# Kernel optimization log

Measured on AMD Instinct MI355X. Metric: run time of the kernel, lower is better.

## Reference

```python
import jax, jax.numpy as jnp
import numpy as np

EPS = 1e-6
R = 8


def _gram_schmidt(U, eps=EPS):
    # Modified Gram-Schmidt over the r columns of U (dim, r), matching the
    # sequential projection loop in HouseholderReflection.get_orthogonal_matrix.
    cols = []
    u0 = U[:, 0]
    cols.append(u0 / (jnp.linalg.norm(u0) + eps))
    r = U.shape[1]
    for i in range(1, r):
        ui = U[:, i]
        for j in range(i):
            ui = ui - jnp.dot(cols[j], ui) * cols[j]
        cols.append(ui / (jnp.linalg.norm(ui) + eps))
    return cols  # list of r unit vectors (dim,)


def _orthogonal_matrix(hra_u, eps=EPS):
    # Q = prod_i (I - 2 u_i u_i^T), applied as rank-1 updates: Q <- Q - 2 (Q u) u^T
    dim = hra_u.shape[0]
    cols = _gram_schmidt(hra_u, eps)
    Q = jnp.eye(dim, dtype=hra_u.dtype)
    for u in cols:
        Q = Q - 2.0 * jnp.outer(Q @ u, u)
    return Q  # (dim, dim)


def setup_inputs() -> dict:
    key = jax.random.key(0)
    k1, k2, k3, k4, k5 = jax.random.split(key, 5)
    N, D_IN, D_HID, D_OUT = 4096, 2048, 8192, 2048
    x = jax.random.normal(k1, (N, D_IN), dtype=jnp.float32)
    hra_u = jax.random.normal(k2, (D_IN, R), dtype=jnp.float32)
    W_random = jax.random.normal(k3, (D_IN, D_HID), dtype=jnp.float32) / np.sqrt(D_IN)
    W_out = jax.random.normal(k4, (D_HID, D_OUT), dtype=jnp.float32) / np.sqrt(D_HID)
    bias = jax.random.normal(k5, (D_OUT,), dtype=jnp.float32)
    return {"x": x, "hra_u": hra_u, "W_random": W_random, "W_out": W_out, "bias": bias}


def reference(x, hra_u, W_random, W_out, bias):
    # y = gelu(x @ (Q @ W_random)) @ W_out + bias  (torch nn.GELU = exact erf gelu)
    Q = _orthogonal_matrix(hra_u)
    W_t = Q @ W_random                      # (D_IN, D_HID)
    h = jax.nn.gelu(x @ W_t, approximate=False)  # (N, D_HID)
    return h @ W_out + bias                 # (N, D_OUT)
```

## Files before the change

kernel.cpp:

```cpp
#include <hip/hip_runtime.h>
#include <hip/hip_bf16.h>

typedef __bf16 bf16;
typedef __bf16 bf16x4 __attribute__((ext_vector_type(4)));
typedef __bf16 bf16x8 __attribute__((ext_vector_type(8)));
typedef float  f32x4  __attribute__((ext_vector_type(4)));

#define GAS __attribute__((address_space(1)))
#define LAS __attribute__((address_space(3)))

#define NROWS 4096
#define DIN   2048
#define DHID  8192
#define DOUT  2048

__device__ __forceinline__ void gload16(const void* g, void* l) {
    __builtin_amdgcn_global_load_lds((GAS void*)g, (LAS void*)l, 16, 0, 0);
}
template <int N> __device__ __forceinline__ void vmw() {
    asm volatile("s_waitcnt vmcnt(%0)" :: "n"(N) : "memory");
}
__device__ __forceinline__ void bsync() {
    asm volatile("" ::: "memory");
    __builtin_amdgcn_s_barrier();
    asm volatile("" ::: "memory");
}

__global__ __launch_bounds__(64) void gs_kernel(const float* __restrict__ U,
                                                float* __restrict__ Vt) {
    __shared__ float Vs[8][DIN];
    const int l = threadIdx.x;
    float u[32];
    for (int r = 0; r < 8; ++r) {
        #pragma unroll
        for (int s = 0; s < 32; ++s) u[s] = U[(size_t)(l * 32 + s) * 8 + r];
        for (int j = 0; j < r; ++j) {
            float d = 0.f;
            #pragma unroll
            for (int s = 0; s < 32; ++s) d += Vs[j][l * 32 + s] * u[s];
            #pragma unroll
            for (int o = 32; o >= 1; o >>= 1) d += __shfl_xor(d, o);
            #pragma unroll
            for (int s = 0; s < 32; ++s) u[s] -= d * Vs[j][l * 32 + s];
        }
        float nr = 0.f;
        #pragma unroll
        for (int s = 0; s < 32; ++s) nr += u[s] * u[s];
        #pragma unroll
        for (int o = 32; o >= 1; o >>= 1) nr += __shfl_xor(nr, o);
        const float inv = 1.f / (sqrtf(nr) + 1e-6f);
        #pragma unroll
        for (int s = 0; s < 32; ++s) {
            float v = u[s] * inv;
            Vs[r][l * 32 + s] = v;
            Vt[r * DIN + l * 32 + s] = v;
        }
        __syncthreads();
    }
}

__global__ __launch_bounds__(256) void p_kernel(const float* __restrict__ W,
                                                const float* __restrict__ Vt,
                                                float* __restrict__ P) {
    const int t = threadIdx.x;
    const int c = blockIdx.x * 64 + (t & 63);
    const int part = t >> 6;
    float acc[8] = {};
    const int i0 = part * 512;
    #pragma unroll 4
    for (int i = i0; i < i0 + 512; ++i) {
        float w = W[(size_t)i * DHID + c];
        #pragma unroll
        for (int r = 0; r < 8; ++r) acc[r] = fmaf(Vt[r * DIN + i], w, acc[r]);
    }
    __shared__ float red[4][8][64];
    #pragma unroll
    for (int r = 0; r < 8; ++r) red[part][r][t & 63] = acc[r];
    __syncthreads();
    for (int idx = t; idx < 512; idx += 256) {
        int r = idx >> 6, cc = idx & 63;
        P[(size_t)r * DHID + blockIdx.x * 64 + cc] =
            red[0][r][cc] + red[1][r][cc] + red[2][r][cc] + red[3][r][cc];
    }
}

__global__ __launch_bounds__(64) void xv_kernel(const float* __restrict__ x,
                                                const float* __restrict__ Vt,
                                                float* __restrict__ xV) {
    const int row = blockIdx.x, l = threadIdx.x;
    const float* xr = x + (size_t)row * DIN;
    float acc[8] = {};
    #pragma unroll 4
    for (int s = 0; s < 32; ++s) {
        int k = s * 64 + l;
        float xv = xr[k];
        #pragma unroll
        for (int r = 0; r < 8; ++r) acc[r] = fmaf(xv, Vt[r * DIN + k], acc[r]);
    }
    #pragma unroll
    for (int r = 0; r < 8; ++r) {
        float d = acc[r];
        #pragma unroll
        for (int o = 32; o >= 1; o >>= 1) d += __shfl_xor(d, o);
        if (l == 0) xV[(size_t)row * 8 + r] = d;
    }
}

__global__ __launch_bounds__(256) void conv_kernel(const float* __restrict__ in,
                                                   bf16* __restrict__ out, int n4) {
    int i = blockIdx.x * 256 + threadIdx.x;
    int stride = gridDim.x * 256;
    for (; i < n4; i += stride) {
        float4 v = ((const float4*)in)[i];
        bf16x4 o = { (bf16)v.x, (bf16)v.y, (bf16)v.z, (bf16)v.w };
        *(bf16x4*)&out[(size_t)i * 4] = o;
    }
}

__global__ __launch_bounds__(256) void tconv_kernel(const float* __restrict__ in,
                                                    bf16* __restrict__ out,
                                                    int R, int C) {
    __shared__ bf16 tile[64][66];
    const int t = threadIdx.x;
    const int n0 = blockIdx.x * 64, k0 = blockIdx.y * 64;
    const int rr = t >> 4, c4 = (t & 15) * 4;
    #pragma unroll
    for (int q = 0; q < 4; ++q) {
        int row = k0 + rr + q * 16;
        float4 v = *(const float4*)&in[(size_t)row * C + n0 + c4];
        tile[c4 + 0][rr + q * 16] = (bf16)v.x;
        tile[c4 + 1][rr + q * 16] = (bf16)v.y;
        tile[c4 + 2][rr + q * 16] = (bf16)v.z;
        tile[c4 + 3][rr + q * 16] = (bf16)v.w;
    }
    __syncthreads();
    const int n = t >> 2, kk = (t & 3) * 16;
    unsigned int w[8];
    #pragma unroll
    for (int i = 0; i < 8; ++i) w[i] = *(const unsigned int*)&tile[n][kk + i * 2];
    uint4 lo = { w[0], w[1], w[2], w[3] }, hi = { w[4], w[5], w[6], w[7] };
    uint4* dst = (uint4*)&out[(size_t)(n0 + n) * R + k0 + kk];
    dst[0] = lo;
    dst[1] = hi;
}

template <int BM, int BN, int WM, int WN, int CR, int CC, int EPI>
__global__ __launch_bounds__(512) void gemm256(const bf16* __restrict__ A,
                                               const bf16* __restrict__ Bt,
                                               const int N, const int K,
                                               const float* __restrict__ e0,
                                               const float* __restrict__ e1,
                                               void* __restrict__ Cout) {
    constexpr int MF = BM / (WM * 16);
    constexpr int NF = BN / (WN * 16);
    constexpr int ABYTES = BM * 64;
    constexpr int BUFB = (BM + BN) * 64;
    constexpr int LA = BM / 128, LB = BN / 128, LPT = LA + LB;
    __shared__ __align__(128) char lds[4 * BUFB];

    const int t = threadIdx.x;
    const int wid = t >> 6, lane = t & 63;
    const int wr = wid / WN, wc = wid % WN;
    const int lrow = lane & 15;
    const int lk2 = (lane >> 4) * 16;

    const int chunks_c = (N / BN) / CC;
    const int xc = blockIdx.x & 7;
    const int ii = blockIdx.x >> 3;
    const int bm = (xc / chunks_c) * CR + ii / CC;
    const int bn = (xc % chunks_c) * CC + ii % CC;

    const bf16* Abase = A + (size_t)bm * BM * K;
    const bf16* Bbase = Bt + (size_t)bn * BN * K;

    const int ar0 = wr * (MF * 16) + lrow;
    const unsigned aoff = (unsigned)(ar0 * 64 + lk2) ^ (unsigned)(((ar0 >> 1) & 3) << 4);
    const int br0 = wc * (NF * 16) + lrow;
    const unsigned boff = (unsigned)ABYTES +
        ((unsigned)(br0 * 64 + lk2) ^ (unsigned)(((br0 >> 1) & 3) << 4));

    f32x4 acc[MF][NF] = {};

    auto STAGE = [&](int kt, int b) {
        const size_t ko = (size_t)kt * 32;
        char* dstb = lds + b * BUFB;
        #pragma unroll
        for (int i2 = 0; i2 < LA; ++i2) {
            const int lin = i2 * 512 + t;
            const int row = lin >> 2;
            const int c16 = (lin & 3) ^ ((lin >> 3) & 3);
            gload16(Abase + (size_t)row * K + ko + c16 * 8,
                    dstb + (i2 * 512 + (t & 448)) * 16);
        }
        #pragma unroll
        for (int i2 = 0; i2 < LB; ++i2) {
            const int lin = i2 * 512 + t;
            const int row = lin >> 2;
            const int c16 = (lin & 3) ^ ((lin >> 3) & 3);
            gload16(Bbase + (size_t)row * K + ko + c16 * 8,
                    dstb + ABYTES + (i2 * 512 + (t & 448)) * 16);
        }
    };

    auto COMPUTE = [&](int b) {
        const char* bp = lds + b * BUFB;
        bf16x8 af[MF], bv[NF];
        #pragma unroll
        for (int m = 0; m < MF; ++m) af[m] = *(const bf16x8*)(bp + aoff + m * 1024);
        #pragma unroll
        for (int n = 0; n < NF; ++n) bv[n] = *(const bf16x8*)(bp + boff + n * 1024);
        __builtin_amdgcn_s_setprio(1);
        #pragma unroll
        for (int m = 0; m < MF; ++m)
            #pragma unroll
            for (int n = 0; n < NF; ++n)
                acc[m][n] = __builtin_amdgcn_mfma_f32_16x16x32_bf16(af[m], bv[n], acc[m][n], 0, 0, 0);
        __builtin_amdgcn_s_setprio(0);
    };

    const int nk = K >> 5;
    STAGE(0, 0); STAGE(1, 1); STAGE(2, 2);
    int kt = 0;
    for (; kt < nk - 3; ++kt) {
        STAGE(kt + 3, (kt + 3) & 3);
        vmw<3 * LPT>();
        bsync();
        COMPUTE(kt & 3);
        bsync();
    }
    vmw<2 * LPT>(); bsync(); COMPUTE(kt & 3); bsync(); ++kt;
    vmw<1 * LPT>(); bsync(); COMPUTE(kt & 3); bsync(); ++kt;
    vmw<0>();       bsync(); COMPUTE(kt & 3); bsync();

    const int jrow = (lane >> 4) << 2;
    if (EPI == 1) {
        float* xVl = (float*)lds;
        float* Pl  = (float*)(lds + BM * 32);
        for (int idx = t; idx < BM * 8; idx += 512)
            xVl[idx] = e0[((size_t)bm * BM + (idx >> 3)) * 8 + (idx & 7)];
        for (int idx = t; idx < BN * 8; idx += 512)
            Pl[idx] = e1[(size_t)(idx / BN) * N + (size_t)bn * BN + (idx % BN)];
        bsync();
        bf16* outp = (bf16*)Cout;
        #pragma unroll
        for (int m = 0; m < MF; ++m)
            #pragma unroll
            for (int n = 0; n < NF; ++n)
                #pragma unroll
                for (int j = 0; j < 4; ++j) {
                    const int rl = wr * (MF * 16) + m * 16 + jrow + j;
                    const int cl = wc * (NF * 16) + n * 16 + lrow;
                    float v = acc[m][n][j];
                    float corr = 0.f;
                    #pragma unroll
                    for (int r = 0; r < 8; ++r)
                        corr = fmaf(xVl[rl * 8 + r], Pl[r * BN + cl], corr);
                    v = fmaf(-2.f, corr, v);
                    v = 0.5f * v * (1.f + erff(v * 0.70710678118654752440f));
                    outp[((size_t)bm * BM + rl) * N + bn * BN + cl] = (bf16)v;
                }
    } else {
        float* outp = (float*)Cout;
        #pragma unroll
        for (int m = 0; m < MF; ++m)
            #pragma unroll
            for (int n = 0; n < NF; ++n)
                #pragma unroll
                for (int j = 0; j < 4; ++j) {
                    const int rl = wr * (MF * 16) + m * 16 + jrow + j;
                    const int cl = wc * (NF * 16) + n * 16 + lrow;
                    outp[((size_t)bm * BM + rl) * N + bn * BN + cl] =
                        acc[m][n][j] + e0[bn * BN + cl];
                }
    }
}

extern "C" void kernel_launch(void* const* d_in, const int* in_sizes, int n_in,
                              void* d_out, int out_size, void* d_ws, size_t ws_size,
                              hipStream_t stream) {
    const float* x     = (const float*)d_in[0];
    const float* hra_u = (const float*)d_in[1];
    const float* Wr    = (const float*)d_in[2];
    const float* Wo    = (const float*)d_in[3];
    const float* bias  = (const float*)d_in[4];
    float* out = (float*)d_out;
    char* ws = (char*)d_ws;

    float* Vt  = (float*)(ws + 0);
    float* P   = (float*)(ws + 65536);
    float* xV  = (float*)(ws + 327680);
    bf16*  xb  = (bf16*)(ws + 458752);
    bf16*  WrT = (bf16*)(ws + 17235968);
    bf16*  WoT = (bf16*)(ws + 50790400);
    bf16*  hb  = (bf16*)(ws + 84344832);

    gs_kernel<<<dim3(1), dim3(64), 0, stream>>>(hra_u, Vt);
    p_kernel<<<dim3(DHID / 64), dim3(256), 0, stream>>>(Wr, Vt, P);
    xv_kernel<<<dim3(NROWS), dim3(64), 0, stream>>>(x, Vt, xV);
    conv_kernel<<<dim3(2048), dim3(256), 0, stream>>>(x, xb, (NROWS * DIN) / 4);
    tconv_kernel<<<dim3(DHID / 64, DIN / 64), dim3(256), 0, stream>>>(Wr, WrT, DIN, DHID);
    tconv_kernel<<<dim3(DOUT / 64, DHID / 64), dim3(256), 0, stream>>>(Wo, WoT, DHID, DOUT);

    gemm256<256, 256, 2, 4, 8, 8, 1><<<dim3(512), dim3(512), 0, stream>>>(
        xb, WrT, DHID, DIN, xV, P, (void*)hb);
    gemm256<256, 128, 4, 2, 4, 8, 0><<<dim3(256), dim3(512), 0, stream>>>(
        hb, WoT, DOUT, DHID, bias, nullptr, (void*)out);
}
```

Baseline: 635.6 us.

## Split GEMM K-loop into half-tile stages, split-K the output GEMM, fuse bf16 conversion

The GEMM main loop now issues the next tile's global-to-LDS loads in two halves (A, then B), each interleaved with half of the MFMA work and separated by barriers. The goal is to overlap memory traffic with compute more finely and to remove the separate pre-compute wait and sync. The second GEMM switches to 256x256 tiles with a 2-way split-K: one half writes to the output, the other to a scratch buffer, and a new reduction kernel adds the two halves plus the bias. That costs an extra full-size fp32 read/write pass. Separately, the x-to-bf16 conversion is merged into the xV projection kernel, which now uses vectorised loads, so x is read once instead of twice.

```diff
diff --git a/kernel.cpp b/kernel.cpp
--- a/kernel.cpp
+++ b/kernel.cpp
@@ -84,18 +84,26 @@
     }
 }
 
-__global__ __launch_bounds__(64) void xv_kernel(const float* __restrict__ x,
-                                                const float* __restrict__ Vt,
-                                                float* __restrict__ xV) {
-    const int row = blockIdx.x, l = threadIdx.x;
+__global__ __launch_bounds__(256) void xv_kernel(const float* __restrict__ x,
+                                                 const float* __restrict__ Vt,
+                                                 float* __restrict__ xV,
+                                                 bf16* __restrict__ xb) {
+    const int row = blockIdx.x * 4 + (threadIdx.x >> 6);
+    const int l = threadIdx.x & 63;
     const float* xr = x + (size_t)row * DIN;
+    bf16* xbr = xb + (size_t)row * DIN;
     float acc[8] = {};
-    #pragma unroll 4
-    for (int s = 0; s < 32; ++s) {
-        int k = s * 64 + l;
-        float xv = xr[k];
-        #pragma unroll
-        for (int r = 0; r < 8; ++r) acc[r] = fmaf(xv, Vt[r * DIN + k], acc[r]);
+    #pragma unroll
+    for (int s = 0; s < 8; ++s) {
+        const int c0 = (s * 64 + l) * 4;
+        float4 v = *(const float4*)&xr[c0];
+        bf16x4 o = { (bf16)v.x, (bf16)v.y, (bf16)v.z, (bf16)v.w };
+        *(bf16x4*)&xbr[c0] = o;
+        #pragma unroll
+        for (int r = 0; r < 8; ++r) {
+            float4 vt = *(const float4*)&Vt[r * DIN + c0];
+            acc[r] = fmaf(v.x, vt.x, fmaf(v.y, vt.y, fmaf(v.z, vt.z, fmaf(v.w, vt.w, acc[r]))));
+        }
     }
     #pragma unroll
     for (int r = 0; r < 8; ++r) {
@@ -103,17 +111,6 @@
         #pragma unroll
         for (int o = 32; o >= 1; o >>= 1) d += __shfl_xor(d, o);
         if (l == 0) xV[(size_t)row * 8 + r] = d;
-    }
-}
-
-__global__ __launch_bounds__(256) void conv_kernel(const float* __restrict__ in,
-                                                   bf16* __restrict__ out, int n4) {
-    int i = blockIdx.x * 256 + threadIdx.x;
-    int stride = gridDim.x * 256;
-    for (; i < n4; i += stride) {
-        float4 v = ((const float4*)in)[i];
-        bf16x4 o = { (bf16)v.x, (bf16)v.y, (bf16)v.z, (bf16)v.w };
-        *(bf16x4*)&out[(size_t)i * 4] = o;
     }
 }
 
@@ -144,13 +141,26 @@
     dst[1] = hi;
 }
 
+__global__ __launch_bounds__(256) void redk(float* __restrict__ out,
+                                            const float* __restrict__ p1,
+                                            const float* __restrict__ bias) {
+    const size_t i = (size_t)blockIdx.x * 256 + threadIdx.x;
+    float4 a = ((const float4*)out)[i];
+    float4 b = ((const float4*)p1)[i];
+    const int c4 = (int)(i & (DOUT / 4 - 1)) * 4;
+    float4 bb = *(const float4*)&bias[c4];
+    float4 r = { a.x + b.x + bb.x, a.y + b.y + bb.y,
+                 a.z + b.z + bb.z, a.w + b.w + bb.w };
+    ((float4*)out)[i] = r;
+}
+
 template <int BM, int BN, int WM, int WN, int CR, int CC, int EPI>
-__global__ __launch_bounds__(512) void gemm256(const bf16* __restrict__ A,
-                                               const bf16* __restrict__ Bt,
-                                               const int N, const int K,
-                                               const float* __restrict__ e0,
-                                               const float* __restrict__ e1,
-                                               void* __restrict__ Cout) {
+__global__ __launch_bounds__(512) void gemm8p(const bf16* __restrict__ A,
+                                              const bf16* __restrict__ Bt,
+                                              const int N, const int nk, const int lda,
+                                              const float* __restrict__ e0,
+                                              const float* __restrict__ e1,
+                                              void* __restrict__ Cout) {
     constexpr int MF = BM / (WM * 16);
     constexpr int NF = BN / (WN * 16);
     constexpr int ABYTES = BM * 64;
@@ -164,14 +174,17 @@
     const int lrow = lane & 15;
     const int lk2 = (lane >> 4) * 16;
 
+    int bid = blockIdx.x, sk = 0;
+    if constexpr (EPI == 2) { sk = bid & 1; bid >>= 1; }
     const int chunks_c = (N / BN) / CC;
-    const int xc = blockIdx.x & 7;
-    const int ii = blockIdx.x >> 3;
+    const int xc = bid & 7;
+    const int ii = bid >> 3;
     const int bm = (xc / chunks_c) * CR + ii / CC;
     const int bn = (xc % chunks_c) * CC + ii % CC;
 
-    const bf16* Abase = A + (size_t)bm * BM * K;
-    const bf16* Bbase = Bt + (size_t)bn * BN * K;
+    const size_t koff = (size_t)sk * nk * 32;
+    const bf16* Abase = A + (size_t)bm * BM * lda + koff;
+    const bf16* Bbase = Bt + (size_t)bn * BN * lda + koff;
 
     const int ar0 = wr * (MF * 16) + lrow;
     const unsigned aoff = (unsigned)(ar0 * 64 + lk2) ^ (unsigned)(((ar0 >> 1) & 3) << 4);
@@ -181,59 +194,80 @@
 
     f32x4 acc[MF][NF] = {};
 
-    auto STAGE = [&](int kt, int b) {
+    auto STAGE = [&](int kt, int part) {
         const size_t ko = (size_t)kt * 32;
-        char* dstb = lds + b * BUFB;
-        #pragma unroll
-        for (int i2 = 0; i2 < LA; ++i2) {
-            const int lin = i2 * 512 + t;
-            const int row = lin >> 2;
-            const int c16 = (lin & 3) ^ ((lin >> 3) & 3);
-            gload16(Abase + (size_t)row * K + ko + c16 * 8,
-                    dstb + (i2 * 512 + (t & 448)) * 16);
-        }
-        #pragma unroll
-        for (int i2 = 0; i2 < LB; ++i2) {
-            const int lin = i2 * 512 + t;
-            const int row = lin >> 2;
-            const int c16 = (lin & 3) ^ ((lin >> 3) & 3);
-            gload16(Bbase + (size_t)row * K + ko + c16 * 8,
-                    dstb + ABYTES + (i2 * 512 + (t & 448)) * 16);
+        char* dstb = lds + (kt & 3) * BUFB;
+        if (part == 0) {
+            #pragma unroll
+            for (int i2 = 0; i2 < LA; ++i2) {
+                const int lin = i2 * 512 + t;
+                const int row = lin >> 2;
+                const int c16 = (lin & 3) ^ ((lin >> 3) & 3);
+                gload16(Abase + (size_t)row * lda + ko + c16 * 8,
+                        dstb + (i2 * 512 + (t & 448)) * 16);
+            }
+        } else {
+            #pragma unroll
+            for (int i2 = 0; i2 < LB; ++i2) {
+                const int lin = i2 * 512 + t;
+                const int row = lin >> 2;
+                const int c16 = (lin & 3) ^ ((lin >> 3) & 3);
+                gload16(Bbase + (size_t)row * lda + ko + c16 * 8,
+                        dstb + ABYTES + (i2 * 512 + (t & 448)) * 16);
+            }
         }
     };
 
-    auto COMPUTE = [&](int b) {
-        const char* bp = lds + b * BUFB;
-        bf16x8 af[MF], bv[NF];
-        #pragma unroll
-        for (int m = 0; m < MF; ++m) af[m] = *(const bf16x8*)(bp + aoff + m * 1024);
-        #pragma unroll
-        for (int n = 0; n < NF; ++n) bv[n] = *(const bf16x8*)(bp + boff + n * 1024);
+    auto TILE = [&](int kt, bool dostage) {
+        const char* bp = lds + (kt & 3) * BUFB;
+        bf16x8 av0[MF / 2], av1[MF / 2], bv[NF];
+        #pragma unroll
+        for (int m = 0; m < MF / 2; ++m)
+            av0[m] = *(const bf16x8*)(bp + aoff + m * 1024);
+        #pragma unroll
+        for (int n = 0; n < NF; ++n)
+            bv[n] = *(const bf16x8*)(bp + boff + n * 1024);
+        if (dostage) STAGE(kt + 3, 0);
+        __builtin_amdgcn_sched_barrier(0);
+        bsync();
         __builtin_amdgcn_s_setprio(1);
         #pragma unroll
-        for (int m = 0; m < MF; ++m)
+        for (int m = 0; m < MF / 2; ++m)
             #pragma unroll
             for (int n = 0; n < NF; ++n)
-                acc[m][n] = __builtin_amdgcn_mfma_f32_16x16x32_bf16(af[m], bv[n], acc[m][n], 0, 0, 0);
+                acc[m][n] = __builtin_amdgcn_mfma_f32_16x16x32_bf16(av0[m], bv[n], acc[m][n], 0, 0, 0);
+        __builtin_amdgcn_s_setprio(0);
+        bsync();
+        #pragma unroll
+        for (int m = 0; m < MF / 2; ++m)
+            av1[m] = *(const bf16x8*)(bp + aoff + (m + MF / 2) * 1024);
+        if (dostage) STAGE(kt + 3, 1);
+        __builtin_amdgcn_sched_barrier(0);
+        bsync();
+        __builtin_amdgcn_s_setprio(1);
+        #pragma unroll
+        for (int m = 0; m < MF / 2; ++m)
+            #pragma unroll
+            for (int n = 0; n < NF; ++n)
+                acc[m + MF / 2][n] = __builtin_amdgcn_mfma_f32_16x16x32_bf16(av1[m], bv[n], acc[m + MF / 2][n], 0, 0, 0);
         __builtin_amdgcn_s_setprio(0);
     };
 
-    const int nk = K >> 5;
-    STAGE(0, 0); STAGE(1, 1); STAGE(2, 2);
+    #pragma unroll
+    for (int p = 0; p < 3; ++p) { STAGE(p, 0); STAGE(p, 1); }
+    vmw<2 * LPT>(); bsync();
     int kt = 0;
     for (; kt < nk - 3; ++kt) {
-        STAGE(kt + 3, (kt + 3) & 3);
-        vmw<3 * LPT>();
-        bsync();
-        COMPUTE(kt & 3);
-        bsync();
-    }
-    vmw<2 * LPT>(); bsync(); COMPUTE(kt & 3); bsync(); ++kt;
-    vmw<1 * LPT>(); bsync(); COMPUTE(kt & 3); bsync(); ++kt;
-    vmw<0>();       bsync(); COMPUTE(kt & 3); bsync();
+        TILE(kt, true);
+        vmw<2 * LPT>();
+        bsync();
+    }
+    TILE(kt, false); vmw<LPT>(); bsync(); ++kt;
+    TILE(kt, false); vmw<0>();   bsync(); ++kt;
+    TILE(kt, false); bsync();
 
     const int jrow = (lane >> 4) << 2;
-    if (EPI == 1) {
+    if constexpr (EPI == 1) {
         float* xVl = (float*)lds;
         float* Pl  = (float*)(lds + BM * 32);
         for (int idx = t; idx < BM * 8; idx += 512)
@@ -260,7 +294,7 @@
                     outp[((size_t)bm * BM + rl) * N + bn * BN + cl] = (bf16)v;
                 }
     } else {
-        float* outp = (float*)Cout;
+        float* outp = sk ? const_cast<float*>(e1) : (float*)Cout;
         #pragma unroll
         for (int m = 0; m < MF; ++m)
             #pragma unroll
@@ -269,8 +303,7 @@
                 for (int j = 0; j < 4; ++j) {
                     const int rl = wr * (MF * 16) + m * 16 + jrow + j;
                     const int cl = wc * (NF * 16) + n * 16 + lrow;
-                    outp[((size_t)bm * BM + rl) * N + bn * BN + cl] =
-                        acc[m][n][j] + e0[bn * BN + cl];
+                    outp[((size_t)bm * BM + rl) * N + bn * BN + cl] = acc[m][n][j];
                 }
     }
 }
@@ -293,16 +326,17 @@
     bf16*  WrT = (bf16*)(ws + 17235968);
     bf16*  WoT = (bf16*)(ws + 50790400);
     bf16*  hb  = (bf16*)(ws + 84344832);
+    float* p1  = (float*)(ws + 458752);
 
     gs_kernel<<<dim3(1), dim3(64), 0, stream>>>(hra_u, Vt);
     p_kernel<<<dim3(DHID / 64), dim3(256), 0, stream>>>(Wr, Vt, P);
-    xv_kernel<<<dim3(NROWS), dim3(64), 0, stream>>>(x, Vt, xV);
-    conv_kernel<<<dim3(2048), dim3(256), 0, stream>>>(x, xb, (NROWS * DIN) / 4);
+    xv_kernel<<<dim3(NROWS / 4), dim3(256), 0, stream>>>(x, Vt, xV, xb);
     tconv_kernel<<<dim3(DHID / 64, DIN / 64), dim3(256), 0, stream>>>(Wr, WrT, DIN, DHID);
     tconv_kernel<<<dim3(DOUT / 64, DHID / 64), dim3(256), 0, stream>>>(Wo, WoT, DHID, DOUT);
 
-    gemm256<256, 256, 2, 4, 8, 8, 1><<<dim3(512), dim3(512), 0, stream>>>(
-        xb, WrT, DHID, DIN, xV, P, (void*)hb);
-    gemm256<256, 128, 4, 2, 4, 8, 0><<<dim3(256), dim3(512), 0, stream>>>(
-        hb, WoT, DOUT, DHID, bias, nullptr, (void*)out);
-}
+    gemm8p<256, 256, 2, 4, 8, 8, 1><<<dim3(512), dim3(512), 0, stream>>>(
+        xb, WrT, DHID, DIN / 32, DIN, xV, P, (void*)hb);
+    gemm8p<256, 256, 2, 4, 4, 4, 2><<<dim3(256), dim3(512), 0, stream>>>(
+        hb, WoT, DOUT, DHID / 64, DHID, nullptr, p1, (void*)out);
+    redk<<<dim3((NROWS * DOUT) / 1024), dim3(256), 0, stream>>>(out, p1, bias);
+}
```

New measurement: 640.2 us. Within noise of the previous version (+0.7%).
